# Kernel tuning notes

Hardware: AMD Instinct MI355X
Metric: run time of the kernel (lower is better)

## Reference

```python
import jax, jax.numpy as jnp
import numpy as np

NUM_CLASSES = 80
TOPK = 100
EPS = 1e-6


def _conv(x, w, b, pad):
    y = jax.lax.conv_general_dilated(
        x, w, window_strides=(1, 1), padding=[(pad, pad), (pad, pad)],
        dimension_numbers=('NCHW', 'OIHW', 'NCHW'))
    return y + b[None, :, None, None]


def _seek_local_maximum(p):
    # 8-neighbor local-maximum test with zero padding, plus >= EPS threshold.
    pp = jnp.pad(p, ((0, 0), (0, 0), (1, 1), (1, 1)))
    m = ((p >= pp[:, :, :-2, 1:-1]) & (p >= pp[:, :, 2:, 1:-1]) &
         (p >= pp[:, :, 1:-1, :-2]) & (p >= pp[:, :, 1:-1, 2:]) &
         (p >= pp[:, :, :-2, :-2]) & (p >= pp[:, :, :-2, 2:]) &
         (p >= pp[:, :, 2:, :-2]) & (p >= pp[:, :, 2:, 2:]) &
         (p >= EPS))
    return m.astype(p.dtype)


def setup_inputs() -> dict:
    key = jax.random.key(0)
    k = jax.random.split(key, 4)
    B, C, H, W = 8, 256, 128, 128
    return {
        'x': jax.random.normal(k[0], (B, C, H, W), jnp.float32),
        'pos_embeddings': jax.random.normal(k[1], (1, C, H, W), jnp.float32),
        'w1': jax.random.normal(k[2], (C, C, 3, 3), jnp.float32) * 0.02,
        'b1': jnp.zeros((C,), jnp.float32),
        'w2': jax.random.normal(k[3], (NUM_CLASSES + 1, C, 1, 1), jnp.float32) * 0.02,
        'b2': jnp.zeros((NUM_CLASSES + 1,), jnp.float32),
    }


def reference(x, pos_embeddings, w1, b1, w2, b2):
    b, c, h, w = x.shape
    # conv3x3 -> relu -> conv1x1 class logits  [b, num_classes+1, h, w]
    logits = _conv(jax.nn.relu(_conv(x, w1, b1, 1)), w2, b2, 0)
    probs = jax.nn.softmax(logits, axis=1)
    # keep only the winning foreground class per pixel (one-hot mask)
    cls_idx = jnp.argmax(probs[:, :NUM_CLASSES], axis=1)  # [b, h, w]
    one_hot = jax.nn.one_hot(cls_idx, NUM_CLASSES + 1, dtype=probs.dtype)
    probs = probs * jnp.transpose(one_hot, (0, 3, 1, 2))
    # boost local maxima (unrolled NMS) then topk over best-class score map
    probs = probs + _seek_local_maximum(probs)
    scores = jnp.max(probs[:, :NUM_CLASSES], axis=1).reshape(b, h * w)
    _, idx = jax.lax.top_k(scores, TOPK)  # [b, TOPK]
    topk_proposals = jnp.take_along_axis(
        x.reshape(b, c, h * w), idx[:, None, :], axis=2)
    pe = jnp.broadcast_to(pos_embeddings, (b,) + pos_embeddings.shape[1:])
    topk_pos_embeddings = jnp.take_along_axis(
        pe.reshape(b, -1, h * w), idx[:, None, :], axis=2)
    # eval mode: topk_locations is None in the original; omit it here
    return topk_proposals, topk_pos_embeddings, logits
```

## Files before the change

### kernel.cpp

```cpp
#include <hip/hip_runtime.h>
#include <cmath>

#define BATCH 8
#define CHN 256
#define HH 128
#define WW 128
#define HWSZ (HH*WW)
#define NCLS 81
#define NFG 80
#define KTOP 100
#define EPSV 1e-6f

typedef __attribute__((ext_vector_type(8))) short short8;
typedef __attribute__((ext_vector_type(4))) float f32x4;

__device__ __forceinline__ ushort f2bf(float f) {
    unsigned u = __float_as_uint(f);
    return (ushort)((u + 0x7FFFu + ((u >> 16) & 1u)) >> 16);
}
__device__ __forceinline__ float bf2f(ushort h) {
    return __uint_as_float(((unsigned)h) << 16);
}

__global__ __launch_bounds__(256) void prep_x(
    const float* __restrict__ x, ushort* __restrict__ xh, ushort* __restrict__ xl)
{
    __shared__ float tile[32][CHN + 1];
    const int blk = blockIdx.x;
    const int q4 = blk & 3, h = (blk >> 2) & 127, b = blk >> 9;
    const int w0 = q4 << 5;
    const int t = threadIdx.x;
    const int px1 = t & 31, cq = t >> 5;

    const float* xb = x + ((size_t)b * CHN) * HWSZ + h * WW + w0;
#pragma unroll 4
    for (int i = 0; i < 32; ++i) {
        int c = i * 8 + cq;
        tile[px1][c] = xb[(size_t)c * HWSZ + px1];
    }
    __syncthreads();
    for (int i = 0; i < 4; ++i) {
        int u = i * 256 + t;
        int c8 = u & 31, px = u >> 5;
        short8 hv, lv;
#pragma unroll
        for (int j = 0; j < 8; ++j) {
            float f = tile[px][c8 * 8 + j];
            ushort hb = f2bf(f);
            hv[j] = (short)hb;
            lv[j] = (short)f2bf(f - bf2f(hb));
        }
        size_t addr = ((size_t)b * HWSZ + h * WW + w0 + px) * CHN + c8 * 8;
        *(short8*)(xh + addr) = hv;
        *(short8*)(xl + addr) = lv;
    }
}

__global__ __launch_bounds__(256) void prep_w(
    const float* __restrict__ w1, const float* __restrict__ w2,
    ushort* __restrict__ Bsw, ushort* __restrict__ w2sw)
{
    int i = blockIdx.x * 256 + threadIdx.x;
    if (i < 73728) {
        int tap  = i >> 13;
        int rem  = i & 8191;
        int kt   = rem >> 10;
        int rem2 = rem & 1023;
        int ntg  = rem2 >> 6;
        int lane = rem2 & 63;
        int oc   = ntg * 16 + (lane & 15);
        int ic0  = kt * 32 + (lane >> 4) * 8;
        size_t base = (size_t)(tap * 8 + kt) * 16384 + (size_t)ntg * 512 + lane * 8;
#pragma unroll
        for (int j = 0; j < 8; ++j) {
            float w  = w1[(size_t)oc * 2304 + (ic0 + j) * 9 + tap];
            ushort hb = f2bf(w);
            Bsw[base + j]        = hb;
            Bsw[base + 8192 + j] = f2bf(w - bf2f(hb));
        }
    } else {
        int j2 = i - 73728;
        int kt   = j2 / 768;
        int rem  = j2 - kt * 768;
        int spl  = rem / 384;
        int rem2 = rem - spl * 384;
        int ntg  = rem2 >> 6;
        int lane = rem2 & 63;
        int oc   = ntg * 16 + (lane & 15);
        int ic0  = kt * 32 + (lane >> 4) * 8;
        size_t base = (size_t)(kt * 12 + spl * 6 + ntg) * 512 + lane * 8;
#pragma unroll
        for (int j = 0; j < 8; ++j) {
            float w = (oc < NCLS) ? w2[(size_t)oc * CHN + ic0 + j] : 0.f;
            ushort hb = f2bf(w);
            w2sw[base + j] = spl ? f2bf(w - bf2f(hb)) : hb;
        }
    }
}

__global__ __launch_bounds__(256, 2) void conv3_mfma2(
    const ushort* __restrict__ xh, const ushort* __restrict__ xl,
    const ushort* __restrict__ Bsw, const float* __restrict__ b1,
    float* __restrict__ y)
{
    __shared__ ushort Ah[3][132 * 32];
    __shared__ ushort Al[3][132 * 32];

    const int blk  = blockIdx.x;
    const int b    = blk >> 7;
    const int h    = blk & 127;
    const int t    = threadIdx.x;
    const int lane = t & 63;
    const int w    = t >> 6;
    const int l15  = lane & 15;
    const int q    = lane >> 4;

    const short8 zz = {0, 0, 0, 0, 0, 0, 0, 0};
    f32x4 acc[8][4];
#pragma unroll
    for (int i = 0; i < 8; ++i)
#pragma unroll
        for (int j = 0; j < 4; ++j) { f32x4 z = {0.f, 0.f, 0.f, 0.f}; acc[i][j] = z; }

    for (int kt = 0; kt < 8; ++kt) {
        __syncthreads();
        for (int u = t; u < 3120; u += 256) {
            int arr = u >= 1560;
            int v   = arr ? u - 1560 : u;
            int kh  = v / 520;
            int r   = v - kh * 520;
            int pxs = r >> 2;
            int qq  = r & 3;
            int gh = h - 1 + kh, gw = pxs - 1;
            short8 val = zz;
            if ((unsigned)gh < (unsigned)HH && (unsigned)gw < (unsigned)WW) {
                const ushort* src = (arr ? xl : xh) +
                    (((size_t)(b * HH + gh) * WW + gw) * CHN + kt * 32 + qq * 8);
                val = *(const short8*)src;
            }
            ushort* dst = (arr ? Al[kh] : Ah[kh]) + pxs * 32 + qq * 8;
            *(short8*)dst = val;
        }
        __syncthreads();

#pragma unroll
        for (int tap = 0; tap < 9; ++tap) {
            const int kh = tap / 3, kw = tap % 3;
            const ushort* bk = Bsw + (size_t)(tap * 8 + kt) * 16384 + lane * 8;
            short8 bh[4], bl[4];
#pragma unroll
            for (int nt = 0; nt < 4; ++nt) {
                bh[nt] = *(const short8*)(bk + (w * 4 + nt) * 512);
                bl[nt] = *(const short8*)(bk + 8192 + (w * 4 + nt) * 512);
            }
#pragma unroll
            for (int mth = 0; mth < 8; mth += 4) {
                short8 ahf[4], alf[4];
#pragma unroll
                for (int mm = 0; mm < 4; ++mm) {
                    int pxs = (mth + mm) * 16 + l15 + kw;
                    ahf[mm] = *(const short8*)(Ah[kh] + pxs * 32 + q * 8);
                    alf[mm] = *(const short8*)(Al[kh] + pxs * 32 + q * 8);
                }
#pragma unroll
                for (int nt = 0; nt < 4; ++nt) {
#pragma unroll
                    for (int mm = 0; mm < 4; ++mm)
                        acc[mth + mm][nt] = __builtin_amdgcn_mfma_f32_16x16x32_bf16(
                            ahf[mm], bh[nt], acc[mth + mm][nt], 0, 0, 0);
#pragma unroll
                    for (int mm = 0; mm < 4; ++mm)
                        acc[mth + mm][nt] = __builtin_amdgcn_mfma_f32_16x16x32_bf16(
                            ahf[mm], bl[nt], acc[mth + mm][nt], 0, 0, 0);
#pragma unroll
                    for (int mm = 0; mm < 4; ++mm)
                        acc[mth + mm][nt] = __builtin_amdgcn_mfma_f32_16x16x32_bf16(
                            alf[mm], bh[nt], acc[mth + mm][nt], 0, 0, 0);
                }
            }
        }
    }

    const size_t rowbase = (size_t)b * HWSZ + h * WW;
#pragma unroll
    for (int nt = 0; nt < 4; ++nt) {
        const int oc = w * 64 + nt * 16 + l15;
        const float bias = b1[oc];
#pragma unroll
        for (int mt = 0; mt < 8; ++mt) {
#pragma unroll
            for (int r = 0; r < 4; ++r) {
                const int px = mt * 16 + q * 4 + r;
                float v = acc[mt][nt][r] + bias;
                y[(rowbase + px) * CHN + oc] = v > 0.f ? v : 0.f;
            }
        }
    }
}

__global__ __launch_bounds__(256) void head_mfma(
    const float* __restrict__ y, const ushort* __restrict__ w2sw,
    const float* __restrict__ b2, float* __restrict__ logits_out,
    int* __restrict__ cls_map, float* __restrict__ prob_map)
{
    __shared__ float ls[128][97];
    const int blk = blockIdx.x;
    const int b = blk >> 7, h = blk & 127;
    const int t = threadIdx.x, lane = t & 63, wm = t >> 6;
    const int l15 = lane & 15, q = lane >> 4;

    f32x4 acc[2][6];
#pragma unroll
    for (int i = 0; i < 2; ++i)
#pragma unroll
        for (int j = 0; j < 6; ++j) { f32x4 z = {0.f, 0.f, 0.f, 0.f}; acc[i][j] = z; }

    const size_t rowbase = (size_t)b * HWSZ + h * WW;

    for (int kt = 0; kt < 8; ++kt) {
        short8 ah[2], al[2];
#pragma unroll
        for (int mt = 0; mt < 2; ++mt) {
            const float* src = y + (rowbase + wm * 32 + mt * 16 + l15) * CHN + kt * 32 + q * 8;
            float4 f0 = *(const float4*)src;
            float4 f1 = *(const float4*)(src + 4);
            float fv[8] = {f0.x, f0.y, f0.z, f0.w, f1.x, f1.y, f1.z, f1.w};
#pragma unroll
            for (int j = 0; j < 8; ++j) {
                ushort hb = f2bf(fv[j]);
                ah[mt][j] = (short)hb;
                al[mt][j] = (short)f2bf(fv[j] - bf2f(hb));
            }
        }
        const ushort* bk = w2sw + (size_t)kt * 12 * 512 + lane * 8;
#pragma unroll
        for (int nt = 0; nt < 6; ++nt) {
            short8 bh = *(const short8*)(bk + nt * 512);
            short8 bl = *(const short8*)(bk + (6 + nt) * 512);
#pragma unroll
            for (int mt = 0; mt < 2; ++mt) {
                acc[mt][nt] = __builtin_amdgcn_mfma_f32_16x16x32_bf16(ah[mt], bh, acc[mt][nt], 0, 0, 0);
                acc[mt][nt] = __builtin_amdgcn_mfma_f32_16x16x32_bf16(ah[mt], bl, acc[mt][nt], 0, 0, 0);
                acc[mt][nt] = __builtin_amdgcn_mfma_f32_16x16x32_bf16(al[mt], bh, acc[mt][nt], 0, 0, 0);
            }
        }
    }

#pragma unroll
    for (int nt = 0; nt < 6; ++nt) {
        const int oc = nt * 16 + l15;
        const float bias = (oc < NCLS) ? b2[oc] : 0.f;
#pragma unroll
        for (int mt = 0; mt < 2; ++mt) {
#pragma unroll
            for (int r = 0; r < 4; ++r) {
                const int px = wm * 32 + mt * 16 + q * 4 + r;
                ls[px][oc] = acc[mt][nt][r] + bias;
            }
        }
    }
    __syncthreads();

    for (int i = t; i < NCLS * 128; i += 256) {
        int c = i >> 7, px = i & 127;
        logits_out[((size_t)b * NCLS + c) * HWSZ + h * WW + px] = ls[px][c];
    }

    if (t < 128) {
        const int px = t;
        float m = -1e30f;
#pragma unroll
        for (int c = 0; c < NCLS; ++c) m = fmaxf(m, ls[px][c]);
        float s = 0.f;
        for (int c = 0; c < NCLS; ++c) s += expf(ls[px][c] - m);
        float best = -1e30f; int bc = 0;
        for (int c = 0; c < NFG; ++c) {
            float v = ls[px][c];
            if (v > best) { best = v; bc = c; }
        }
        cls_map[rowbase + px]  = bc;
        prob_map[rowbase + px] = expf(best - m) / s;
    }
}

__global__ __launch_bounds__(256) void locmax_kernel(
    const int* __restrict__ cls_map, const float* __restrict__ prob_map,
    float* __restrict__ score)
{
    int i = blockIdx.x * 256 + threadIdx.x;
    int b = i >> 14;
    int p = i & (HWSZ - 1);
    int h = p >> 7, w = p & 127;
    int mycls = cls_map[i];
    float myp = prob_map[i];
    bool lm = (myp >= EPSV);
#pragma unroll
    for (int dh = -1; dh <= 1; ++dh)
#pragma unroll
        for (int dw = -1; dw <= 1; ++dw) {
            if (dh == 0 && dw == 0) continue;
            int nh = h + dh, nw = w + dw;
            if ((unsigned)nh < HH && (unsigned)nw < WW) {
                int ni = b * HWSZ + nh * WW + nw;
                if (cls_map[ni] == mycls && myp < prob_map[ni]) lm = false;
            }
        }
    score[i] = myp + (lm ? 1.f : 0.f);
}

__global__ __launch_bounds__(1024) void topk_kernel(
    const float* __restrict__ score, int* __restrict__ idx_out)
{
    __shared__ unsigned int hist[256];
    __shared__ unsigned long long cand[2048];
    __shared__ unsigned int sprefix, sneed, scntA, scntB;
    const int b = blockIdx.x;
    const int t = threadIdx.x;
    const float* sc = score + b * HWSZ;

    unsigned keys[16];
#pragma unroll
    for (int i = 0; i < 16; ++i)
        keys[i] = __float_as_uint(sc[t + (i << 10)]);

    if (t == 0) { sneed = KTOP; sprefix = 0; scntA = 0; scntB = 0; }

    for (int lvl = 0; lvl < 4; ++lvl) {
        const int shift = 24 - 8 * lvl;
        if (t < 256) hist[t] = 0;
        __syncthreads();
        const unsigned pref = sprefix;
#pragma unroll
        for (int i = 0; i < 16; ++i) {
            unsigned k = keys[i];
            bool match = (lvl == 0) || ((k >> (shift + 8)) == pref);
            if (match) atomicAdd(&hist[(k >> shift) & 255u], 1u);
        }
        __syncthreads();
        if (t == 0) {
            unsigned needv = sneed, c = 0; int bsel = 0;
            for (int j = 255; j >= 0; --j) {
                unsigned nc = c + hist[j];
                if (nc >= needv) { bsel = j; break; }
                c = nc;
            }
            sprefix = (pref << 8) | (unsigned)bsel;
            sneed = needv - c;
        }
        __syncthreads();
    }

    const unsigned K = sprefix;
#pragma unroll
    for (int i = 0; i < 16; ++i) {
        unsigned k = keys[i];
        int p = t + (i << 10);
        if (k > K) {
            unsigned pos = atomicAdd(&scntA, 1u);
            cand[pos] = ((unsigned long long)k << 32) | (unsigned)(~p);
        } else if (k == K) {
            unsigned pos = atomicAdd(&scntB, 1u);
            if (pos < 1920u)
                cand[128 + pos] = ((unsigned long long)k << 32) | (unsigned)(~p);
        }
    }
    __syncthreads();
    const int cA = (int)scntA;
    const int cB = (int)(scntB < 1920u ? scntB : 1920u);
    const int Ctot = cA + cB;
    for (int ti = t; ti < Ctot; ti += 1024) {
        unsigned long long my = cand[ti < cA ? ti : 128 + (ti - cA)];
        int rank = 0;
        for (int j = 0; j < Ctot; ++j) {
            unsigned long long o = cand[j < cA ? j : 128 + (j - cA)];
            rank += (o > my) ? 1 : 0;
        }
        if (rank < KTOP)
            idx_out[b * KTOP + rank] =
                (int)(~(unsigned)(my & 0xFFFFFFFFull)) & (HWSZ - 1);
    }
}

__global__ __launch_bounds__(256) void gather_kernel(
    const float* __restrict__ x, const float* __restrict__ pos,
    const int* __restrict__ idx, float* __restrict__ out0,
    float* __restrict__ out1)
{
    int blk = blockIdx.x;
    int b = blk / KTOP;
    int j = blk - b * KTOP;
    int c = threadIdx.x;
    int pix = idx[b * KTOP + j];
    out0[((size_t)b * CHN + c) * KTOP + j] = x[((size_t)b * CHN + c) * HWSZ + pix];
    out1[((size_t)b * CHN + c) * KTOP + j] = pos[(size_t)c * HWSZ + pix];
}

extern "C" void kernel_launch(void* const* d_in, const int* in_sizes, int n_in,
                              void* d_out, int out_size, void* d_ws, size_t ws_size,
                              hipStream_t stream) {
    (void)in_sizes; (void)n_in; (void)out_size; (void)ws_size;
    const float* x   = (const float*)d_in[0];
    const float* pos = (const float*)d_in[1];
    const float* w1  = (const float*)d_in[2];
    const float* b1  = (const float*)d_in[3];
    const float* w2  = (const float*)d_in[4];
    const float* b2  = (const float*)d_in[5];

    float* out0   = (float*)d_out;
    float* out1   = out0 + BATCH * CHN * KTOP;
    float* logits = out1 + BATCH * CHN * KTOP;

    char* ws = (char*)d_ws;
    const size_t NPX = (size_t)BATCH * HWSZ;

    size_t off = 0;
    int*    cls_map  = (int*)(ws + off);    off += NPX * 4;
    float*  prob_map = (float*)(ws + off);  off += NPX * 4;
    float*  score    = (float*)(ws + off);  off += NPX * 4;
    int*    idx      = (int*)(ws + off);    off += 4096;
    ushort* w2sw     = (ushort*)(ws + off); off += (size_t)8 * 12 * 512 * 2;
    ushort* Bsw      = (ushort*)(ws + off); off += (size_t)9 * 8 * 16384 * 2;
    ushort* xh       = (ushort*)(ws + off); off += NPX * CHN * 2;
    ushort* xl       = (ushort*)(ws + off); off += NPX * CHN * 2;
    float*  y        = (float*)(ws + off);  off += NPX * CHN * 4;

    prep_x<<<4096, 256, 0, stream>>>(x, xh, xl);
    prep_w<<<312, 256, 0, stream>>>(w1, w2, Bsw, w2sw);
    conv3_mfma2<<<1024, 256, 0, stream>>>(xh, xl, Bsw, b1, y);
    head_mfma<<<1024, 256, 0, stream>>>(y, w2sw, b2, logits, cls_map, prob_map);
    locmax_kernel<<<(int)(NPX / 256), 256, 0, stream>>>(cls_map, prob_map, score);
    topk_kernel<<<BATCH, 1024, 0, stream>>>(score, idx);
    gather_kernel<<<BATCH * KTOP, 256, 0, stream>>>(x, pos, idx, out0, out1);
}
```

Measured before the change: 774.0 us.

## Pipeline conv3x3 input staging with direct global-to-LDS loads and swizzled layout

Restructures the 3x3 conv kernel so the input is staged one kernel row at a time (24 stages over channel tiles and kh), and the next stage is issued with global_load_lds while MFMAs run on the current stage. The shared-memory layout is XOR-swizzled to reduce bank conflicts, and border columns are zeroed once. The block-to-(b,h) mapping is changed so neighbouring blocks share rows, and s_setprio is raised around the MFMA bursts. The 3-slot ring buffer relies on a single barrier per stage, so writes into a slot that is still being read are a correctness risk.

```diff
diff --git a/kernel.cpp b/kernel.cpp
--- a/kernel.cpp
+++ b/kernel.cpp
@@ -20,6 +20,12 @@
 }
 __device__ __forceinline__ float bf2f(ushort h) {
     return __uint_as_float(((unsigned)h) << 16);
+}
+
+__device__ __forceinline__ void gl16(const void* g, void* l) {
+    __builtin_amdgcn_global_load_lds(
+        (const __attribute__((address_space(1))) void*)g,
+        (__attribute__((address_space(3))) void*)l, 16, 0, 0);
 }
 
 __global__ __launch_bounds__(256) void prep_x(
@@ -98,23 +104,34 @@
     }
 }
 
-__global__ __launch_bounds__(256, 2) void conv3_mfma2(
+__global__ __launch_bounds__(256, 2) void conv3_pipe(
     const ushort* __restrict__ xh, const ushort* __restrict__ xl,
     const ushort* __restrict__ Bsw, const float* __restrict__ b1,
     float* __restrict__ y)
 {
-    __shared__ ushort Ah[3][132 * 32];
-    __shared__ ushort Al[3][132 * 32];
+    __shared__ ushort A[3][2][132 * 32];
 
     const int blk  = blockIdx.x;
-    const int b    = blk >> 7;
-    const int h    = blk & 127;
+    const int b    = blk & 7;
+    const int h    = blk >> 3;
     const int t    = threadIdx.x;
     const int lane = t & 63;
     const int w    = t >> 6;
     const int l15  = lane & 15;
     const int q    = lane >> 4;
 
+    int colb[4], ldsu[4], basew[4];
+#pragma unroll
+    for (int r = 0; r < 4; ++r) {
+        int e   = (r * 256 + t) & 511;
+        int pxs = (e >> 2) + 1;
+        int qq  = e & 3;
+        int qs  = qq ^ ((pxs >> 1) & 3);
+        colb[r]  = (pxs - 1) * CHN + qs * 8;
+        ldsu[r]  = pxs * 32 + qq * 8;
+        basew[r] = ((((r * 256 + (t & 192)) & 511) >> 2) + 1) * 32;
+    }
+
     const short8 zz = {0, 0, 0, 0, 0, 0, 0, 0};
     f32x4 acc[8][4];
 #pragma unroll
@@ -122,30 +139,40 @@
 #pragma unroll
         for (int j = 0; j < 4; ++j) { f32x4 z = {0.f, 0.f, 0.f, 0.f}; acc[i][j] = z; }
 
-    for (int kt = 0; kt < 8; ++kt) {
-        __syncthreads();
-        for (int u = t; u < 3120; u += 256) {
-            int arr = u >= 1560;
-            int v   = arr ? u - 1560 : u;
-            int kh  = v / 520;
-            int r   = v - kh * 520;
-            int pxs = r >> 2;
-            int qq  = r & 3;
-            int gh = h - 1 + kh, gw = pxs - 1;
-            short8 val = zz;
-            if ((unsigned)gh < (unsigned)HH && (unsigned)gw < (unsigned)WW) {
-                const ushort* src = (arr ? xl : xh) +
-                    (((size_t)(b * HH + gh) * WW + gw) * CHN + kt * 32 + qq * 8);
-                val = *(const short8*)src;
-            }
-            ushort* dst = (arr ? Al[kh] : Ah[kh]) + pxs * 32 + qq * 8;
-            *(short8*)dst = val;
-        }
-        __syncthreads();
-
-#pragma unroll
-        for (int tap = 0; tap < 9; ++tap) {
-            const int kh = tap / 3, kw = tap % 3;
+    if (t < 96) {
+        int sl = t >> 5, rr = t & 31, arr = rr >> 4, pp = (rr >> 2) & 3, qq = rr & 3;
+        int pxs = pp ? 128 + pp : 0;
+        *(short8*)&A[sl][arr][pxs * 32 + qq * 8] = zz;
+    }
+
+    auto stage = [&](int sn) {
+        int kt1 = sn / 3;
+        int kh1 = sn - kt1 * 3;
+        int gh  = h - 1 + kh1;
+        if ((unsigned)gh < (unsigned)HH) {
+            size_t rowb = ((size_t)(b * HH + gh) * WW) * CHN + kt1 * 32;
+#pragma unroll
+            for (int r = 0; r < 4; ++r) {
+                const ushort* g = (r < 2 ? xh : xl) + rowb + colb[r];
+                gl16(g, &A[kh1][r >> 1][basew[r]]);
+            }
+        } else {
+#pragma unroll
+            for (int r = 0; r < 4; ++r)
+                *(short8*)&A[kh1][r >> 1][ldsu[r]] = zz;
+        }
+    };
+
+    stage(0);
+    __syncthreads();
+
+#pragma unroll 1
+    for (int s = 0; s < 24; ++s) {
+        const int kt = s / 3;
+        const int kh = s - kt * 3;
+#pragma unroll
+        for (int kw = 0; kw < 3; ++kw) {
+            const int tap = kh * 3 + kw;
             const ushort* bk = Bsw + (size_t)(tap * 8 + kt) * 16384 + lane * 8;
             short8 bh[4], bl[4];
 #pragma unroll
@@ -153,15 +180,18 @@
                 bh[nt] = *(const short8*)(bk + (w * 4 + nt) * 512);
                 bl[nt] = *(const short8*)(bk + 8192 + (w * 4 + nt) * 512);
             }
+            if (kw == 0 && s < 23) stage(s + 1);
 #pragma unroll
             for (int mth = 0; mth < 8; mth += 4) {
                 short8 ahf[4], alf[4];
 #pragma unroll
                 for (int mm = 0; mm < 4; ++mm) {
                     int pxs = (mth + mm) * 16 + l15 + kw;
-                    ahf[mm] = *(const short8*)(Ah[kh] + pxs * 32 + q * 8);
-                    alf[mm] = *(const short8*)(Al[kh] + pxs * 32 + q * 8);
+                    int cof = pxs * 32 + ((q ^ ((pxs >> 1) & 3)) * 8);
+                    ahf[mm] = *(const short8*)&A[kh][0][cof];
+                    alf[mm] = *(const short8*)&A[kh][1][cof];
                 }
+                __builtin_amdgcn_s_setprio(1);
 #pragma unroll
                 for (int nt = 0; nt < 4; ++nt) {
 #pragma unroll
@@ -177,8 +207,10 @@
                         acc[mth + mm][nt] = __builtin_amdgcn_mfma_f32_16x16x32_bf16(
                             alf[mm], bh[nt], acc[mth + mm][nt], 0, 0, 0);
                 }
-            }
-        }
+                __builtin_amdgcn_s_setprio(0);
+            }
+        }
+        __syncthreads();
     }
 
     const size_t rowbase = (size_t)b * HWSZ + h * WW;
@@ -426,7 +458,7 @@
 
     prep_x<<<4096, 256, 0, stream>>>(x, xh, xl);
     prep_w<<<312, 256, 0, stream>>>(w1, w2, Bsw, w2sw);
-    conv3_mfma2<<<1024, 256, 0, stream>>>(xh, xl, Bsw, b1, y);
+    conv3_pipe<<<1024, 256, 0, stream>>>(xh, xl, Bsw, b1, y);
     head_mfma<<<1024, 256, 0, stream>>>(y, w2sw, b2, logits, cls_map, prob_map);
     locmax_kernel<<<(int)(NPX / 256), 256, 0, stream>>>(cls_map, prob_map, score);
     topk_kernel<<<BATCH, 1024, 0, stream>>>(score, idx);
```

Result: faster. 716.6 us (-7.4%).
